# Kernel optimization log

Hardware: AMD Instinct MI355X
Metric: run time of the kernel (lower is better)

## Reference

```python
import jax, jax.numpy as jnp
import numpy as np

KLD_BINS = 10
RATIO_KLD = 0.5
# categorical one-hot blocks in the 99-dim Adult encoding
BLOCKS = [(1, 8), (8, 24), (24, 31), (31, 45), (45, 51), (51, 53), (53, 55), (58, 99)]
CONT_COLS = np.array([0, 55, 56, 57])


def _cross_entropy(logits, onehot):
    # F.cross_entropy with targets = argmax of the one-hot block (mean over batch)
    logp = jax.nn.log_softmax(logits, axis=-1)
    return -jnp.mean(jnp.sum(onehot * logp, axis=-1))


def _kl_divergence(p, q):
    # np-style KL: sum p*log(p/q) over valid (nonzero) bins
    valid = (p > 0) & (q > 0)
    ratio = jnp.where(valid, p / jnp.where(valid, q, 1.0), 1.0)
    return jnp.sum(jnp.where(valid, p * jnp.log(ratio), 0.0))


def setup_inputs() -> dict:
    B = 262144
    key = jax.random.key(0)
    ks = jax.random.split(key, 16)
    data_decoded = jax.random.normal(ks[0], (B, 99), dtype=jnp.float32)
    # data_true: continuous columns + one-hot categorical blocks
    data_true = jnp.zeros((B, 99), dtype=jnp.float32)
    data_true = data_true.at[:, CONT_COLS].set(jax.random.normal(ks[1], (B, 4), dtype=jnp.float32))
    for j, (s, e) in enumerate(BLOCKS):
        lab = jax.random.randint(ks[2 + j], (B,), 0, e - s)
        data_true = data_true.at[:, s:e].set(jax.nn.one_hot(lab, e - s, dtype=jnp.float32))
    data_encoded = jax.random.normal(ks[11], (B, 12), dtype=jnp.float32)
    sex = jax.random.bernoulli(ks[12], 0.5, (B,)).astype(jnp.float32)
    data_encoded = data_encoded.at[:, 11].set(sex)  # column 11 of combined is the 0/1 sex neuron
    label_true = jax.random.normal(ks[13], (B, 2), dtype=jnp.float32)
    return {
        'data_encoded': data_encoded,
        'data_decoded': data_decoded,
        'data_true': data_true,
        'label_true': label_true,
        'batch_size': B,
    }


def reference(data_encoded, data_decoded, data_true, label_true, batch_size):
    # --- reconstruction MSE on continuous columns ---
    cc = jnp.asarray(CONT_COLS)
    mse_loss = jnp.sum(jnp.mean((data_decoded[:, cc] - data_true[:, cc]) ** 2, axis=0))
    # --- cross-entropy on each categorical block ---
    ce_loss = jnp.float32(0.0)
    for s, e in BLOCKS:
        ce_loss = ce_loss + _cross_entropy(data_decoded[:, s:e], data_true[:, s:e])
    # --- per-feature histogram KLD between male/female groups (no grad, as in torch via .numpy()) ---
    comb = jnp.concatenate([data_encoded, label_true], axis=1)  # [B, 14]
    feats = comb[:, :KLD_BINS]  # first 10 encoded features, [B, 10]
    mn = jnp.min(feats, axis=0)  # per-column min over full batch (torch .item())
    mx = jnp.max(feats, axis=0)
    width = jnp.maximum(mx - mn, 1e-12)
    # torch.histc bin index: floor((x-min)/(max-min)*bins), x==max -> last bin
    idx = jnp.clip(jnp.floor((feats - mn) / width * KLD_BINS).astype(jnp.int32), 0, KLD_BINS - 1)
    onehot = jax.nn.one_hot(idx, KLD_BINS, dtype=jnp.float32)  # [B, 10, bins]
    sexcol = comb[:, 11]
    m_mask = (sexcol == 0).astype(jnp.float32)
    f_mask = (sexcol == 1).astype(jnp.float32)
    m_count = jnp.maximum(jnp.sum(m_mask), 1.0)
    f_count = jnp.maximum(jnp.sum(f_mask), 1.0)
    m_hist = jnp.einsum('b,bik->ik', m_mask, onehot) / m_count  # [10, bins]
    f_hist = jnp.einsum('b,bik->ik', f_mask, onehot) / f_count
    kld = jax.lax.stop_gradient(_kl_divergence(m_hist, f_hist))
    alpha = RATIO_KLD
    multi_loss = (1.0 - alpha) * (mse_loss + ce_loss) + alpha * kld
    return (multi_loss, mse_loss, ce_loss, alpha * kld)
```

## Files before the change

kernel.cpp:

```cpp
#include <hip/hip_runtime.h>
#include <math.h>

#define B_ROWS 262144

#define WS_A 0
#define WS_B 2816
#define WS_C 28416
#define MAIN_BLOCKS 768
#define N_WAVES (MAIN_BLOCKS * 4)
#define TILE_ROWS 16
#define N_TILES 16384
#define TILE_F4 396

__device__ __forceinline__ unsigned int map_f(float x) {
  unsigned int b = __float_as_uint(x);
  return (b & 0x80000000u) ? ~b : (b | 0x80000000u);
}
__device__ __forceinline__ float unmap_f(unsigned int u) {
  unsigned int b = (u & 0x80000000u) ? (u ^ 0x80000000u) : ~u;
  return __uint_as_float(b);
}

__global__ __launch_bounds__(256) void k_minmax(const float* __restrict__ enc,
                                                unsigned int* __restrict__ ws) {
  int tid = threadIdx.x, bid = blockIdx.x;
  const float4* e4 = (const float4*)enc;
  float mn[10], mx[10];
  #pragma unroll
  for (int j = 0; j < 10; j++) { mn[j] = 1e30f; mx[j] = -1e30f; }
  unsigned int cm = 0, cf = 0;
  #pragma unroll
  for (int i = 0; i < 8; i++) {
    size_t g = (size_t)bid * 2048 + i * 256 + tid;
    float4 a = e4[g * 3 + 0], b = e4[g * 3 + 1], c = e4[g * 3 + 2];
    float v[12] = {a.x,a.y,a.z,a.w,b.x,b.y,b.z,b.w,c.x,c.y,c.z,c.w};
    #pragma unroll
    for (int j = 0; j < 10; j++) { mn[j] = fminf(mn[j], v[j]); mx[j] = fmaxf(mx[j], v[j]); }
    cm += (v[11] == 0.0f); cf += (v[11] == 1.0f);
  }
  #pragma unroll
  for (int off = 32; off; off >>= 1) {
    #pragma unroll
    for (int j = 0; j < 10; j++) {
      mn[j] = fminf(mn[j], __shfl_xor(mn[j], off));
      mx[j] = fmaxf(mx[j], __shfl_xor(mx[j], off));
    }
    cm += __shfl_xor(cm, off); cf += __shfl_xor(cf, off);
  }
  __shared__ float smn[4][10], smx[4][10];
  __shared__ unsigned int sc[4][2];
  int wave = tid >> 6, lane = tid & 63;
  if (lane == 0) {
    #pragma unroll
    for (int j = 0; j < 10; j++) { smn[wave][j] = mn[j]; smx[wave][j] = mx[j]; }
    sc[wave][0] = cm; sc[wave][1] = cf;
  }
  __syncthreads();
  unsigned int* out = ws + WS_A + bid * 22;
  if (tid < 10) {
    float m = fminf(fminf(smn[0][tid], smn[1][tid]), fminf(smn[2][tid], smn[3][tid]));
    out[tid] = map_f(m);
  } else if (tid < 20) {
    int j = tid - 10;
    float m = fmaxf(fmaxf(smx[0][j], smx[1][j]), fmaxf(smx[2][j], smx[3][j]));
    out[tid] = map_f(m);
  } else if (tid < 22) {
    int j = tid - 20;
    out[tid] = sc[0][j] + sc[1][j] + sc[2][j] + sc[3][j];
  }
}

__global__ __launch_bounds__(256) void k_hist(const float* __restrict__ enc,
                                              unsigned int* __restrict__ ws) {
  __shared__ float mnv[10], wid[10];
  __shared__ unsigned int h[200];
  int tid = threadIdx.x, bid = blockIdx.x;
  for (int i = tid; i < 200; i += 256) h[i] = 0u;
  if (tid < 10) {
    unsigned int umn = 0xFFFFFFFFu, umx = 0u;
    #pragma unroll 4
    for (int b = 0; b < 128; b++) {
      umn = min(umn, ws[WS_A + b * 22 + tid]);
      umx = max(umx, ws[WS_A + b * 22 + 10 + tid]);
    }
    float mn = unmap_f(umn);
    mnv[tid] = mn;
    wid[tid] = fmaxf(unmap_f(umx) - mn, 1e-12f);
  }
  __syncthreads();
  const float4* e4 = (const float4*)enc;
  #pragma unroll
  for (int i = 0; i < 8; i++) {
    size_t g = (size_t)bid * 2048 + i * 256 + tid;
    float4 a = e4[g * 3 + 0], b = e4[g * 3 + 1], c = e4[g * 3 + 2];
    float v[12] = {a.x,a.y,a.z,a.w,b.x,b.y,b.z,b.w,c.x,c.y,c.z,c.w};
    int base = (v[11] == 0.0f) ? 0 : ((v[11] == 1.0f) ? 100 : -1);
    if (base >= 0) {
      #pragma unroll
      for (int cc = 0; cc < 10; cc++) {
        float t = (v[cc] - mnv[cc]) / wid[cc] * 10.0f;
        int bi = min(max((int)floorf(t), 0), 9);
        atomicAdd(&h[base + cc * 10 + bi], 1u);
      }
    }
  }
  __syncthreads();
  if (tid < 200) ws[WS_B + bid * 200 + tid] = h[tid];
}

__global__ __launch_bounds__(256) void k_main(const float* __restrict__ d,
                                              const float* __restrict__ t,
                                              unsigned int* __restrict__ ws) {
  __shared__ float sd[4 * 3168];
  __shared__ float st[4 * 3168];
  int tid = threadIdx.x, bid = blockIdx.x;
  int wave = tid >> 6, lane = tid & 63;
  float* ldsd = sd + wave * 3168;
  float* ldst = st + wave * 3168;
  const float4* ld4 = (const float4*)ldsd;
  const float4* lt4 = (const float4*)ldst;
  int gw = bid * 4 + wave;

  float mse = 0.f, dot = 0.f, ce = 0.f;

  for (int tile = gw; tile < N_TILES; tile += N_WAVES) {
    const float4* ds = (const float4*)d + (size_t)tile * TILE_F4;
    const float4* ts = (const float4*)t + (size_t)tile * TILE_F4;
    #pragma unroll
    for (int it = 0; it < 6; ++it)
      __builtin_amdgcn_global_load_lds(
          (const __attribute__((address_space(1))) void*)(ds + it * 64 + lane),
          (__attribute__((address_space(3))) void*)(ldsd + it * 1024 / 4), 16, 0, 0);
    if (lane < 12)
      __builtin_amdgcn_global_load_lds(
          (const __attribute__((address_space(1))) void*)(ds + 384 + lane),
          (__attribute__((address_space(3))) void*)(ldsd + 1536), 16, 0, 0);
    #pragma unroll
    for (int it = 0; it < 6; ++it)
      __builtin_amdgcn_global_load_lds(
          (const __attribute__((address_space(1))) void*)(ts + it * 64 + lane),
          (__attribute__((address_space(3))) void*)(ldst + it * 1024 / 4), 16, 0, 0);
    if (lane < 12)
      __builtin_amdgcn_global_load_lds(
          (const __attribute__((address_space(1))) void*)(ts + 384 + lane),
          (__attribute__((address_space(3))) void*)(ldst + 1536), 16, 0, 0);

    asm volatile("s_waitcnt vmcnt(0)" ::: "memory");

    #pragma unroll
    for (int it = 0; it < 7; ++it) {
      int f = it * 64 + lane;
      if (f < TILE_F4) {
        float4 xd = ld4[f];
        float4 xt = lt4[f];
        int e = f * 4;
        int c = e - (e / 99) * 99;
        float dv[4] = {xd.x, xd.y, xd.z, xd.w};
        float tv[4] = {xt.x, xt.y, xt.z, xt.w};
        #pragma unroll
        for (int k = 0; k < 4; k++) {
          int cc = c + k;
          if (cc >= 99) cc -= 99;
          bool cont = (cc == 0) | ((unsigned)(cc - 55) <= 2u);
          float diff = dv[k] - tv[k];
          if (cont) mse += diff * diff;
          else      dot += tv[k] * dv[k];
        }
      }
    }
    if (lane < TILE_ROWS) {
      const float* row = ldsd + lane * 99;
      float Z;
      Z = 0.f;
      #pragma unroll
      for (int c = 1; c < 8; c++) Z += __expf(row[c]);
      ce += __logf(Z);
      Z = 0.f;
      #pragma unroll
      for (int c = 8; c < 24; c++) Z += __expf(row[c]);
      ce += __logf(Z);
      Z = 0.f;
      #pragma unroll
      for (int c = 24; c < 31; c++) Z += __expf(row[c]);
      ce += __logf(Z);
      Z = 0.f;
      #pragma unroll
      for (int c = 31; c < 45; c++) Z += __expf(row[c]);
      ce += __logf(Z);
      Z = 0.f;
      #pragma unroll
      for (int c = 45; c < 51; c++) Z += __expf(row[c]);
      ce += __logf(Z);
      Z = 0.f;
      #pragma unroll
      for (int c = 51; c < 53; c++) Z += __expf(row[c]);
      ce += __logf(Z);
      Z = 0.f;
      #pragma unroll
      for (int c = 53; c < 55; c++) Z += __expf(row[c]);
      ce += __logf(Z);
      Z = 0.f;
      #pragma unroll
      for (int c = 58; c < 99; c++) Z += __expf(row[c]);
      ce += __logf(Z);
    }
    asm volatile("s_waitcnt lgkmcnt(0)" ::: "memory");
  }

  #pragma unroll
  for (int off = 32; off; off >>= 1) {
    mse += __shfl_xor(mse, off);
    dot += __shfl_xor(dot, off);
    ce  += __shfl_xor(ce,  off);
  }
  if (lane == 0) {
    float* C = (float*)(ws + WS_C);
    C[gw]               = mse;
    C[N_WAVES + gw]     = dot;
    C[2 * N_WAVES + gw] = ce;
  }
}

__global__ __launch_bounds__(256) void k_final(const unsigned int* __restrict__ ws,
                                               float* __restrict__ out) {
  __shared__ float h[200];
  __shared__ float part[256];
  __shared__ float red3[12];
  __shared__ float cnts[2];
  int tid = threadIdx.x;
  if (tid < 200) {
    unsigned int s = 0;
    #pragma unroll 4
    for (int b = 0; b < 128; b++) s += ws[WS_B + b * 200 + tid];
    h[tid] = (float)s;
  }
  if (tid == 200 || tid == 201) {
    unsigned int s = 0;
    #pragma unroll 4
    for (int b = 0; b < 128; b++) s += ws[WS_A + b * 22 + 20 + (tid - 200)];
    cnts[tid - 200] = fmaxf((float)s, 1.0f);
  }
  const float* C = (const float*)(ws + WS_C);
  float msum = 0.f, dsum = 0.f, csum = 0.f;
  for (int i = tid; i < N_WAVES; i += 256) {
    msum += C[i]; dsum += C[N_WAVES + i]; csum += C[2 * N_WAVES + i];
  }
  #pragma unroll
  for (int off = 32; off; off >>= 1) {
    msum += __shfl_xor(msum, off);
    dsum += __shfl_xor(dsum, off);
    csum += __shfl_xor(csum, off);
  }
  int wave = tid >> 6, lane = tid & 63;
  if (lane == 0) { red3[wave] = msum; red3[4 + wave] = dsum; red3[8 + wave] = csum; }
  __syncthreads();
  float term = 0.f;
  if (tid < 100) {
    float mc = h[tid], fc = h[100 + tid];
    if (mc > 0.f && fc > 0.f) {
      float p = mc / cnts[0];
      float q = fc / cnts[1];
      term = p * logf(p / q);
    }
  }
  part[tid] = term;
  __syncthreads();
  for (int s = 128; s; s >>= 1) {
    if (tid < s) part[tid] += part[tid + s];
    __syncthreads();
  }
  if (tid == 0) {
    const float invB = 1.0f / (float)B_ROWS;
    float mse = (red3[0] + red3[1] + red3[2] + red3[3]) * invB;
    float dd  = (red3[4] + red3[5] + red3[6] + red3[7]);
    float cc  = (red3[8] + red3[9] + red3[10] + red3[11]);
    float ce  = (cc - dd) * invB;
    float akld = 0.5f * part[0];
    out[0] = 0.5f * (mse + ce) + akld;
    out[1] = mse;
    out[2] = ce;
    out[3] = akld;
  }
}

extern "C" void kernel_launch(void* const* d_in, const int* in_sizes, int n_in,
                              void* d_out, int out_size, void* d_ws, size_t ws_size,
                              hipStream_t stream) {
  const float* enc = (const float*)d_in[0];
  const float* dec = (const float*)d_in[1];
  const float* tru = (const float*)d_in[2];
  unsigned int* ws = (unsigned int*)d_ws;
  float* out = (float*)d_out;

  hipLaunchKernelGGL(k_minmax, dim3(128),         dim3(256), 0, stream, enc, ws);
  hipLaunchKernelGGL(k_hist,   dim3(128),         dim3(256), 0, stream, enc, ws);
  hipLaunchKernelGGL(k_main,   dim3(MAIN_BLOCKS), dim3(256), 0, stream, dec, tru, ws);
  hipLaunchKernelGGL(k_final,  dim3(1),           dim3(256), 0, stream, ws, out);
}
```

Measured before the change: 271.3 us.

## Halve tile size, load target directly to registers, split CE across lane pairs

The main kernel now processes 8-row tiles with twice as many blocks and declares a minimum of 6 blocks per CU in its launch bounds. Only the decoded data is staged in LDS; the target tile is loaded straight into registers, which cuts LDS use per block. The cross-entropy work is split across two lanes per row to shorten the serial exp/log chain. Per-block partials are reduced in shared memory before writing, so the final kernel reads fewer values. The risk is more loop iterations with smaller transfers each, plus register pressure from the occupancy hint.

Result: no change. 270.0 us (-0.5%).

```diff
diff --git a/kernel.cpp b/kernel.cpp
--- a/kernel.cpp
+++ b/kernel.cpp
@@ -6,11 +6,11 @@
 #define WS_A 0
 #define WS_B 2816
 #define WS_C 28416
-#define MAIN_BLOCKS 768
+#define MAIN_BLOCKS 1536
 #define N_WAVES (MAIN_BLOCKS * 4)
-#define TILE_ROWS 16
-#define N_TILES 16384
-#define TILE_F4 396
+#define TILE_ROWS 8
+#define N_TILES 32768
+#define TILE_F4 198
 
 __device__ __forceinline__ unsigned int map_f(float x) {
   unsigned int b = __float_as_uint(x);
@@ -108,17 +108,15 @@
   if (tid < 200) ws[WS_B + bid * 200 + tid] = h[tid];
 }
 
-__global__ __launch_bounds__(256) void k_main(const float* __restrict__ d,
-                                              const float* __restrict__ t,
-                                              unsigned int* __restrict__ ws) {
-  __shared__ float sd[4 * 3168];
-  __shared__ float st[4 * 3168];
+__global__ __launch_bounds__(256, 6) void k_main(const float* __restrict__ d,
+                                                 const float* __restrict__ t,
+                                                 unsigned int* __restrict__ ws) {
+  __shared__ float sd[4][800];
+  __shared__ float red[12];
   int tid = threadIdx.x, bid = blockIdx.x;
   int wave = tid >> 6, lane = tid & 63;
-  float* ldsd = sd + wave * 3168;
-  float* ldst = st + wave * 3168;
+  float* ldsd = sd[wave];
   const float4* ld4 = (const float4*)ldsd;
-  const float4* lt4 = (const float4*)ldst;
   int gw = bid * 4 + wave;
 
   float mse = 0.f, dot = 0.f, ce = 0.f;
@@ -127,84 +125,81 @@
     const float4* ds = (const float4*)d + (size_t)tile * TILE_F4;
     const float4* ts = (const float4*)t + (size_t)tile * TILE_F4;
     #pragma unroll
-    for (int it = 0; it < 6; ++it)
+    for (int it = 0; it < 3; ++it)
       __builtin_amdgcn_global_load_lds(
           (const __attribute__((address_space(1))) void*)(ds + it * 64 + lane),
-          (__attribute__((address_space(3))) void*)(ldsd + it * 1024 / 4), 16, 0, 0);
-    if (lane < 12)
+          (__attribute__((address_space(3))) void*)(ldsd + it * 256), 16, 0, 0);
+    if (lane < 6)
       __builtin_amdgcn_global_load_lds(
-          (const __attribute__((address_space(1))) void*)(ds + 384 + lane),
-          (__attribute__((address_space(3))) void*)(ldsd + 1536), 16, 0, 0);
-    #pragma unroll
-    for (int it = 0; it < 6; ++it)
-      __builtin_amdgcn_global_load_lds(
-          (const __attribute__((address_space(1))) void*)(ts + it * 64 + lane),
-          (__attribute__((address_space(3))) void*)(ldst + it * 1024 / 4), 16, 0, 0);
-    if (lane < 12)
-      __builtin_amdgcn_global_load_lds(
-          (const __attribute__((address_space(1))) void*)(ts + 384 + lane),
-          (__attribute__((address_space(3))) void*)(ldst + 1536), 16, 0, 0);
-
+          (const __attribute__((address_space(1))) void*)(ds + 192 + lane),
+          (__attribute__((address_space(3))) void*)(ldsd + 768), 16, 0, 0);
+    float4 tv0 = ts[lane];
+    float4 tv1 = ts[64 + lane];
+    float4 tv2 = ts[128 + lane];
+    float4 tv3 = (lane < 6) ? ts[192 + lane] : make_float4(0.f, 0.f, 0.f, 0.f);
     asm volatile("s_waitcnt vmcnt(0)" ::: "memory");
 
-    #pragma unroll
-    for (int it = 0; it < 7; ++it) {
+    float4 tvv[4] = {tv0, tv1, tv2, tv3};
+    #pragma unroll
+    for (int it = 0; it < 4; ++it) {
       int f = it * 64 + lane;
       if (f < TILE_F4) {
         float4 xd = ld4[f];
-        float4 xt = lt4[f];
+        float4 xt = tvv[it];
         int e = f * 4;
         int c = e - (e / 99) * 99;
         float dv[4] = {xd.x, xd.y, xd.z, xd.w};
-        float tv[4] = {xt.x, xt.y, xt.z, xt.w};
+        float tw[4] = {xt.x, xt.y, xt.z, xt.w};
         #pragma unroll
         for (int k = 0; k < 4; k++) {
           int cc = c + k;
           if (cc >= 99) cc -= 99;
           bool cont = (cc == 0) | ((unsigned)(cc - 55) <= 2u);
-          float diff = dv[k] - tv[k];
+          float diff = dv[k] - tw[k];
           if (cont) mse += diff * diff;
-          else      dot += tv[k] * dv[k];
+          else      dot += tw[k] * dv[k];
         }
       }
     }
-    if (lane < TILE_ROWS) {
-      const float* row = ldsd + lane * 99;
+    if (lane < 2 * TILE_ROWS) {
+      const float* row = ldsd + (lane >> 1) * 99;
       float Z;
-      Z = 0.f;
-      #pragma unroll
-      for (int c = 1; c < 8; c++) Z += __expf(row[c]);
-      ce += __logf(Z);
-      Z = 0.f;
-      #pragma unroll
-      for (int c = 8; c < 24; c++) Z += __expf(row[c]);
-      ce += __logf(Z);
-      Z = 0.f;
-      #pragma unroll
-      for (int c = 24; c < 31; c++) Z += __expf(row[c]);
-      ce += __logf(Z);
-      Z = 0.f;
-      #pragma unroll
-      for (int c = 31; c < 45; c++) Z += __expf(row[c]);
-      ce += __logf(Z);
-      Z = 0.f;
-      #pragma unroll
-      for (int c = 45; c < 51; c++) Z += __expf(row[c]);
-      ce += __logf(Z);
-      Z = 0.f;
-      #pragma unroll
-      for (int c = 51; c < 53; c++) Z += __expf(row[c]);
-      ce += __logf(Z);
-      Z = 0.f;
-      #pragma unroll
-      for (int c = 53; c < 55; c++) Z += __expf(row[c]);
-      ce += __logf(Z);
-      Z = 0.f;
-      #pragma unroll
-      for (int c = 58; c < 99; c++) Z += __expf(row[c]);
-      ce += __logf(Z);
-    }
-    asm volatile("s_waitcnt lgkmcnt(0)" ::: "memory");
+      if ((lane & 1) == 0) {
+        Z = 0.f;
+        #pragma unroll
+        for (int c = 1; c < 8; c++) Z += __expf(row[c]);
+        ce += __logf(Z);
+        Z = 0.f;
+        #pragma unroll
+        for (int c = 8; c < 24; c++) Z += __expf(row[c]);
+        ce += __logf(Z);
+        Z = 0.f;
+        #pragma unroll
+        for (int c = 24; c < 31; c++) Z += __expf(row[c]);
+        ce += __logf(Z);
+        Z = 0.f;
+        #pragma unroll
+        for (int c = 31; c < 45; c++) Z += __expf(row[c]);
+        ce += __logf(Z);
+        Z = 0.f;
+        #pragma unroll
+        for (int c = 45; c < 51; c++) Z += __expf(row[c]);
+        ce += __logf(Z);
+      } else {
+        Z = 0.f;
+        #pragma unroll
+        for (int c = 51; c < 53; c++) Z += __expf(row[c]);
+        ce += __logf(Z);
+        Z = 0.f;
+        #pragma unroll
+        for (int c = 53; c < 55; c++) Z += __expf(row[c]);
+        ce += __logf(Z);
+        Z = 0.f;
+        #pragma unroll
+        for (int c = 58; c < 99; c++) Z += __expf(row[c]);
+        ce += __logf(Z);
+      }
+    }
   }
 
   #pragma unroll
@@ -213,11 +208,13 @@
     dot += __shfl_xor(dot, off);
     ce  += __shfl_xor(ce,  off);
   }
-  if (lane == 0) {
+  if (lane == 0) { red[wave] = mse; red[4 + wave] = dot; red[8 + wave] = ce; }
+  __syncthreads();
+  if (tid == 0) {
     float* C = (float*)(ws + WS_C);
-    C[gw]               = mse;
-    C[N_WAVES + gw]     = dot;
-    C[2 * N_WAVES + gw] = ce;
+    C[bid]                   = red[0] + red[1] + red[2]  + red[3];
+    C[MAIN_BLOCKS + bid]     = red[4] + red[5] + red[6]  + red[7];
+    C[2 * MAIN_BLOCKS + bid] = red[8] + red[9] + red[10] + red[11];
   }
 }
 
@@ -242,8 +239,8 @@
   }
   const float* C = (const float*)(ws + WS_C);
   float msum = 0.f, dsum = 0.f, csum = 0.f;
-  for (int i = tid; i < N_WAVES; i += 256) {
-    msum += C[i]; dsum += C[N_WAVES + i]; csum += C[2 * N_WAVES + i];
+  for (int i = tid; i < MAIN_BLOCKS; i += 256) {
+    msum += C[i]; dsum += C[MAIN_BLOCKS + i]; csum += C[2 * MAIN_BLOCKS + i];
   }
   #pragma unroll
   for (int off = 32; off; off >>= 1) {
```
